# Kernel optimization log

Hardware: AMD Instinct MI355X
Metric: run time of the kernel (lower is better)

## Reference

```python
import jax, jax.numpy as jnp
import numpy as np

D_MODEL = 1024
N_HEADS = 16
HEAD_DIM = 64
SEQ = 2048
BATCH = 2
NEG = -1e9


def rotate_half(t):
    t1, t2 = jnp.split(t, 2, axis=-1)
    return jnp.concatenate([-t2, t1], axis=-1)


def setup_inputs() -> dict:
    key = jax.random.key(0)
    ks = jax.random.split(key, 7)
    std = 0.02
    x = jax.random.normal(ks[0], (BATCH, SEQ, D_MODEL), dtype=jnp.float32)
    # RoPE tables [seq_len, head_dim]
    inv_freq = 1.0 / (10000.0 ** (jnp.arange(0, HEAD_DIM, 2, dtype=jnp.float32) / HEAD_DIM))
    t = jnp.arange(SEQ, dtype=jnp.float32)
    freqs = jnp.outer(t, inv_freq)
    emb = jnp.concatenate([freqs, freqs], axis=-1)
    cos = jnp.cos(emb)
    sin = jnp.sin(emb)
    Wq = std * jax.random.normal(ks[1], (D_MODEL, D_MODEL), dtype=jnp.float32)
    Wk = std * jax.random.normal(ks[2], (D_MODEL, D_MODEL), dtype=jnp.float32)
    Wv = std * jax.random.normal(ks[3], (D_MODEL, D_MODEL), dtype=jnp.float32)
    Wo = std * jax.random.normal(ks[4], (D_MODEL, D_MODEL), dtype=jnp.float32)
    return {"x": x, "cos": cos, "sin": sin, "Wq": Wq, "Wk": Wk, "Wv": Wv, "Wo": Wo}


def reference(x, cos, sin, Wq, Wk, Wv, Wo):
    B, S, _ = x.shape
    scale = 1.0 / np.sqrt(HEAD_DIM)
    # projections (nn.Linear: y = x @ W.T)
    q = (x @ Wq.T).reshape(B, S, N_HEADS, HEAD_DIM).transpose(0, 2, 1, 3)  # [B,H,S,D]
    k = (x @ Wk.T).reshape(B, S, N_HEADS, HEAD_DIM).transpose(0, 2, 1, 3)
    v = (x @ Wv.T).reshape(B, S, N_HEADS, HEAD_DIM).transpose(0, 2, 1, 3)
    # RoPE
    c = cos[None, None, :, :]
    s = sin[None, None, :, :]
    q = q * c + rotate_half(q) * s
    k = k * c + rotate_half(k) * s
    # attention with additive causal mask
    scores = jnp.einsum('bhqd,bhkd->bhqk', q, k) * scale
    causal = jnp.triu(jnp.ones((S, S), dtype=jnp.float32), k=1) * NEG
    scores = scores + causal[None, None]
    attn = jax.nn.softmax(scores, axis=-1)
    out = jnp.einsum('bhqk,bhkd->bhqd', attn, v)
    out = out.transpose(0, 2, 1, 3).reshape(B, S, D_MODEL)
    return out @ Wo.T
```

## Files before the change

kernel.cpp:

```cpp
#include <hip/hip_runtime.h>
#include <hip/hip_bf16.h>
#include <math.h>

#define DM    1024
#define SEQL  2048
#define NB    2
#define MTOT  4096

typedef __attribute__((ext_vector_type(8))) short short8;
typedef __attribute__((ext_vector_type(4))) short short4v;
typedef __attribute__((ext_vector_type(4))) float float4v;

#define GLDS16(g, l) __builtin_amdgcn_global_load_lds( \
    (const __attribute__((address_space(1))) void*)(g), \
    (__attribute__((address_space(3))) void*)(l), 16, 0, 0)

__device__ __forceinline__ short f2bf(float f) {
  union { float f; unsigned u; } c; c.f = f;
  unsigned r = c.u + 0x7FFFu + ((c.u >> 16) & 1u);
  return (short)(r >> 16);
}

__device__ __forceinline__ int packbf(float a, float b) {
  union { float f; unsigned u; } ca, cb; ca.f = a; cb.f = b;
  return (int)__builtin_amdgcn_perm(cb.u + 0x8000u, ca.u + 0x8000u, 0x07060302u);
}

__global__ __launch_bounds__(256) void cvt_all(
    const float* __restrict__ x, const float* __restrict__ wq, const float* __restrict__ wk,
    const float* __restrict__ wv, const float* __restrict__ wo,
    short* __restrict__ xb, short* __restrict__ wqb, short* __restrict__ wkb,
    short* __restrict__ wvb, short* __restrict__ wob) {
  const int n4x = MTOT * DM / 4;
  int i = blockIdx.x * 256 + threadIdx.x;
  const float* s; short* d; int off;
  if (i < n4x) { s = x; d = xb; off = i; }
  else {
    int j = i - n4x;
    int sel = j >> 18;
    off = j & 0x3FFFF;
    s = (sel == 0) ? wq : (sel == 1) ? wk : (sel == 2) ? wv : wo;
    d = (sel == 0) ? wqb : (sel == 1) ? wkb : (sel == 2) ? wvb : wob;
  }
  float4 v = ((const float4*)s)[off];
  short4v o;
  o.x = f2bf(v.x); o.y = f2bf(v.y); o.z = f2bf(v.z); o.w = f2bf(v.w);
  ((short4v*)d)[off] = o;
}

__global__ __launch_bounds__(256, 3) void qkv_kernel(
    const short* __restrict__ A,
    const short* __restrict__ B0, const short* __restrict__ B1, const short* __restrict__ B2,
    short* __restrict__ out0, short* __restrict__ out1, short* __restrict__ out2,
    const float* __restrict__ cosp, const float* __restrict__ sinp)
{
  __shared__ short As[128 * 32];
  __shared__ short Bs[128 * 32];
  const int t = threadIdx.x;
  const int w = t >> 6, lane = t & 63;
  const int quad = lane >> 4, l16 = lane & 15;
  const int wm = w >> 1, wn = w & 1;
  const int bm = blockIdx.y * 128, bn = blockIdx.x * 128;

  const short* Bw = (blockIdx.z == 0) ? B0 : ((blockIdx.z == 1) ? B1 : B2);

  float4v acc[4][4];
#pragma unroll
  for (int i = 0; i < 4; ++i)
#pragma unroll
    for (int j = 0; j < 4; ++j) { float4v z = {0.f, 0.f, 0.f, 0.f}; acc[i][j] = z; }

  for (int k0 = 0; k0 < DM; k0 += 32) {
#pragma unroll
    for (int i = 0; i < 2; ++i) {
      const int c = i * 256 + t;
      const int row = c >> 2, kc = c & 3;
      GLDS16(A  + (size_t)(bm + row) * DM + k0 + kc * 8, As + (i * 256 + w * 64) * 8);
      GLDS16(Bw + (size_t)(bn + row) * DM + k0 + kc * 8, Bs + (i * 256 + w * 64) * 8);
    }
    __syncthreads();
    short8 af[4], bf[4];
#pragma unroll
    for (int mt = 0; mt < 4; ++mt) af[mt] = *(const short8*)&As[(wm * 64 + mt * 16 + l16) * 32 + quad * 8];
#pragma unroll
    for (int nt = 0; nt < 4; ++nt) bf[nt] = *(const short8*)&Bs[(wn * 64 + nt * 16 + l16) * 32 + quad * 8];
#pragma unroll
    for (int mt = 0; mt < 4; ++mt)
#pragma unroll
      for (int nt = 0; nt < 4; ++nt)
        acc[mt][nt] = __builtin_amdgcn_mfma_f32_16x16x32_bf16(af[mt], bf[nt], acc[mt][nt], 0, 0, 0);
    __syncthreads();
  }

  if (blockIdx.z < 2) {
    short* qo = (blockIdx.z == 0) ? out0 : out1;
    const float sc = (blockIdx.z == 0) ? 0.18033688011112042f : 1.0f;
#pragma unroll
    for (int mt = 0; mt < 4; ++mt)
#pragma unroll
      for (int r = 0; r < 4; ++r) {
        int grow = bm + wm * 64 + mt * 16 + quad * 4 + r;
        int s = grow & (SEQL - 1);
        int base = grow * DM + bn + wn * 64;
#pragma unroll
        for (int nt = 0; nt < 2; ++nt) {
          int d1 = nt * 16 + l16;
          float q1 = acc[mt][nt][r], q2 = acc[mt][nt + 2][r];
          float c1 = cosp[s * 64 + d1] * sc,      s1 = sinp[s * 64 + d1] * sc;
          float c2 = cosp[s * 64 + 32 + d1] * sc, s2 = sinp[s * 64 + 32 + d1] * sc;
          qo[base + d1]      = f2bf(q1 * c1 - q2 * s1);
          qo[base + 32 + d1] = f2bf(q2 * c2 + q1 * s2);
        }
      }
  } else {
    short* vo = out2;
#pragma unroll
    for (int mt = 0; mt < 4; ++mt)
#pragma unroll
      for (int nt = 0; nt < 4; ++nt) {
        int gc = bn + wn * 64 + nt * 16 + l16;
        int g0 = bm + wm * 64 + mt * 16 + quad * 4;
        short4v pk;
#pragma unroll
        for (int r = 0; r < 4; ++r) pk[r] = f2bf(acc[mt][nt][r]);
        *(short4v*)&vo[(size_t)gc * MTOT + g0] = pk;
      }
  }
}

#if __has_builtin(__builtin_amdgcn_mfma_f32_16x16x16bf16_1k)
#define HAVE_MFMA16 1
#define MFMA16(a, b, c) __builtin_amdgcn_mfma_f32_16x16x16bf16_1k(a, b, c, 0, 0, 0)
#else
#define HAVE_MFMA16 0
#endif

__global__ __launch_bounds__(256, 2) void attn_kernel(
    const short* __restrict__ Q, const short* __restrict__ K,
    const short* __restrict__ Vt, short* __restrict__ O)
{
  __shared__ short Ks[128 * 64];
  __shared__ short Vs[64 * 128];
  const int t = threadIdx.x;
  const int w = t >> 6, lane = t & 63;
  const int quad = lane >> 4, l16 = lane & 15;
  const int qtA = blockIdx.x;
  const int qtB = 31 - blockIdx.x;
  const int bh = blockIdx.y;
  const int b = bh >> 4, h = bh & 15;
  const int rowbase = b * SEQL;
  const int colbase = h * 64;
  const int nktA = (qtA >> 1) + 1;
  const int nktB = (qtB >> 1) + 1;
  const int qA = qtA * 64 + w * 16 + l16;
  const int qB = qtB * 64 + w * 16 + l16;

  short8 aqA[2], aqB[2];
#pragma unroll
  for (int kk = 0; kk < 2; ++kk) {
    aqA[kk] = *(const short8*)&Q[(size_t)(rowbase + qA) * DM + colbase + kk * 32 + quad * 8];
    aqB[kk] = *(const short8*)&Q[(size_t)(rowbase + qB) * DM + colbase + kk * 32 + quad * 8];
  }

  float4v odA[4], odB[4];
#pragma unroll
  for (int j = 0; j < 4; ++j) { float4v z = {0.f, 0.f, 0.f, 0.f}; odA[j] = z; odB[j] = z; }
  float lA = 0.f, lB = 0.f;

  for (int kt = 0; kt < nktB; ++kt) {
    const bool actA = (kt < nktA);
    const bool diagA = (kt == nktA - 1), diagB = (kt == nktB - 1);
    {
      const short* Kbase = K + (size_t)(rowbase + kt * 128) * DM + colbase;
      const short* Vbase = Vt + (size_t)colbase * MTOT + rowbase + kt * 128;
#pragma unroll
      for (int j = 0; j < 4; ++j) {
        int i = j * 256 + t;
        int n = i >> 3, c = (i & 7) ^ (n & 7);
        GLDS16(Kbase + (size_t)n * DM + c * 8, Ks + (j * 256 + w * 64) * 8);
      }
#pragma unroll
      for (int j = 0; j < 4; ++j) {
        int i = j * 256 + t;
        int d = i >> 4, c = (i & 15) ^ (d & 7);
        GLDS16(Vbase + (size_t)d * MTOT + c * 8, Vs + (j * 256 + w * 64) * 8);
      }
    }
    __syncthreads();

    int pkA[8][2], pkB[8][2];
#pragma unroll
    for (int nt = 0; nt < 8; ++nt) {
      int n = nt * 16 + l16;
      short8 bk0 = *(const short8*)&Ks[(n * 8 + (quad ^ (n & 7))) * 8];
      short8 bk1 = *(const short8*)&Ks[(n * 8 + ((4 + quad) ^ (n & 7))) * 8];
      const int kb = kt * 128 + nt * 16 + quad * 4;
      float4v zz = {0.f, 0.f, 0.f, 0.f};
      float4v sB = __builtin_amdgcn_mfma_f32_16x16x32_bf16(bk0, aqB[0], zz, 0, 0, 0);
      sB = __builtin_amdgcn_mfma_f32_16x16x32_bf16(bk1, aqB[1], sB, 0, 0, 0);
      float pb[4];
#pragma unroll
      for (int r = 0; r < 4; ++r) {
        float p = (diagB && (kb + r > qB)) ? 0.f : __builtin_amdgcn_exp2f(sB[r]);
        lB += p; pb[r] = p;
      }
      pkB[nt][0] = packbf(pb[0], pb[1]);
      pkB[nt][1] = packbf(pb[2], pb[3]);
      if (actA) {
        float4v sA = __builtin_amdgcn_mfma_f32_16x16x32_bf16(bk0, aqA[0], zz, 0, 0, 0);
        sA = __builtin_amdgcn_mfma_f32_16x16x32_bf16(bk1, aqA[1], sA, 0, 0, 0);
        float pa[4];
#pragma unroll
        for (int r = 0; r < 4; ++r) {
          float p = (diagA && (kb + r > qA)) ? 0.f : __builtin_amdgcn_exp2f(sA[r]);
          lA += p; pa[r] = p;
        }
        pkA[nt][0] = packbf(pa[0], pa[1]);
        pkA[nt][1] = packbf(pa[2], pa[3]);
      }
    }

#if HAVE_MFMA16
#pragma unroll
    for (int kk = 0; kk < 8; ++kk) {
      union { int i[2]; short4v s; } ubB, ubA;
      ubB.i[0] = pkB[kk][0]; ubB.i[1] = pkB[kk][1];
      if (actA) { ubA.i[0] = pkA[kk][0]; ubA.i[1] = pkA[kk][1]; }
#pragma unroll
      for (int dt = 0; dt < 4; ++dt) {
        int d = dt * 16 + l16;
        short4v av = *(const short4v*)&Vs[(d * 16 + ((kk * 2 + (quad >> 1)) ^ (d & 7))) * 8 + (quad & 1) * 4];
        odB[dt] = MFMA16(av, ubB.s, odB[dt]);
        if (actA) odA[dt] = MFMA16(av, ubA.s, odA[dt]);
      }
    }
#else
#pragma unroll
    for (int kk = 0; kk < 4; ++kk) {
      union { int i[4]; short8 s; } ubB, ubA;
#pragma unroll
      for (int dj = 0; dj < 4; ++dj) {
        int src = (((quad & 1) * 2 + (dj >> 1)) << 4) + l16;
        int b0 = __shfl(pkB[2 * kk][dj & 1], src);
        int b1 = __shfl(pkB[2 * kk + 1][dj & 1], src);
        ubB.i[dj] = (quad >= 2) ? b1 : b0;
        int a0 = __shfl(pkA[2 * kk][dj & 1], src);
        int a1 = __shfl(pkA[2 * kk + 1][dj & 1], src);
        ubA.i[dj] = (quad >= 2) ? a1 : a0;
      }
#pragma unroll
      for (int dt = 0; dt < 4; ++dt) {
        int d = dt * 16 + l16;
        short8 av = *(const short8*)&Vs[(d * 16 + ((kk * 4 + quad) ^ (d & 7))) * 8];
        odB[dt] = __builtin_amdgcn_mfma_f32_16x16x32_bf16(av, ubB.s, odB[dt], 0, 0, 0);
        if (actA) odA[dt] = __builtin_amdgcn_mfma_f32_16x16x32_bf16(av, ubA.s, odA[dt], 0, 0, 0);
      }
    }
#endif
    __syncthreads();
  }

  lA += __shfl_xor(lA, 16); lA += __shfl_xor(lA, 32);
  lB += __shfl_xor(lB, 16); lB += __shfl_xor(lB, 32);
  const float iA = 1.f / lA, iB = 1.f / lB;

#pragma unroll
  for (int dt = 0; dt < 4; ++dt) {
    short4v sa, sb;
#pragma unroll
    for (int r = 0; r < 4; ++r) { sa[r] = f2bf(odA[dt][r] * iA); sb[r] = f2bf(odB[dt][r] * iB); }
    int col = colbase + dt * 16 + quad * 4;
    *(short4v*)&O[(size_t)(rowbase + qA) * DM + col] = sa;
    *(short4v*)&O[(size_t)(rowbase + qB) * DM + col] = sb;
  }
}

__global__ __launch_bounds__(256, 2) void gemm_out(
    const short* __restrict__ A, const short* __restrict__ B,
    float* __restrict__ out)
{
  __shared__ short As[128 * 32];
  __shared__ short Bs[64 * 32];
  const int t = threadIdx.x;
  const int w = t >> 6, lane = t & 63;
  const int quad = lane >> 4, l16 = lane & 15;
  const int wm = w >> 1, wn = w & 1;
  const int bm = blockIdx.y * 128, bn = blockIdx.x * 64;

  float4v acc[4][2];
#pragma unroll
  for (int i = 0; i < 4; ++i)
#pragma unroll
    for (int j = 0; j < 2; ++j) { float4v z = {0.f, 0.f, 0.f, 0.f}; acc[i][j] = z; }

  for (int k0 = 0; k0 < DM; k0 += 32) {
#pragma unroll
    for (int i = 0; i < 2; ++i) {
      const int c = i * 256 + t;
      const int row = c >> 2, kc = c & 3;
      GLDS16(A + (size_t)(bm + row) * DM + k0 + kc * 8, As + (i * 256 + w * 64) * 8);
    }
    {
      const int row = t >> 2, kc = t & 3;
      GLDS16(B + (size_t)(bn + row) * DM + k0 + kc * 8, Bs + (w * 64) * 8);
    }
    __syncthreads();
    short8 af[4], bf[2];
#pragma unroll
    for (int mt = 0; mt < 4; ++mt) af[mt] = *(const short8*)&As[(wm * 64 + mt * 16 + l16) * 32 + quad * 8];
#pragma unroll
    for (int nt = 0; nt < 2; ++nt) bf[nt] = *(const short8*)&Bs[(wn * 32 + nt * 16 + l16) * 32 + quad * 8];
#pragma unroll
    for (int mt = 0; mt < 4; ++mt)
#pragma unroll
      for (int nt = 0; nt < 2; ++nt)
        acc[mt][nt] = __builtin_amdgcn_mfma_f32_16x16x32_bf16(af[mt], bf[nt], acc[mt][nt], 0, 0, 0);
    __syncthreads();
  }

#pragma unroll
  for (int mt = 0; mt < 4; ++mt)
#pragma unroll
    for (int nt = 0; nt < 2; ++nt)
#pragma unroll
      for (int r = 0; r < 4; ++r) {
        int grow = bm + wm * 64 + mt * 16 + quad * 4 + r;
        int gcol = bn + wn * 32 + nt * 16 + l16;
        out[(size_t)grow * DM + gcol] = acc[mt][nt][r];
      }
}

extern "C" void kernel_launch(void* const* d_in, const int* in_sizes, int n_in,
                              void* d_out, int out_size, void* d_ws, size_t ws_size,
                              hipStream_t stream) {
  const float* x    = (const float*)d_in[0];
  const float* cosp = (const float*)d_in[1];
  const float* sinp = (const float*)d_in[2];
  const float* Wq   = (const float*)d_in[3];
  const float* Wk   = (const float*)d_in[4];
  const float* Wv   = (const float*)d_in[5];
  const float* Wo   = (const float*)d_in[6];

  char* ws = (char*)d_ws;
  const size_t XB = (size_t)MTOT * DM * 2;
  const size_t WB = (size_t)DM * DM * 2;
  short* xb    = (short*)(ws);
  short* wqb   = (short*)(ws + XB);
  short* wkb   = (short*)(ws + XB + 1 * WB);
  short* wvb   = (short*)(ws + XB + 2 * WB);
  short* wob   = (short*)(ws + XB + 3 * WB);
  short* Qb    = (short*)(ws + XB + 4 * WB);
  short* Kb    = (short*)(ws + XB + 4 * WB + XB);
  short* Vtb   = (short*)(ws + XB + 4 * WB + 2 * XB);
  short* attnb = xb;

  const int n4tot = (MTOT * DM + 4 * DM * DM) / 4;
  hipLaunchKernelGGL(cvt_all, dim3(n4tot / 256), dim3(256), 0, stream,
                     x, Wq, Wk, Wv, Wo, xb, wqb, wkb, wvb, wob);

  hipLaunchKernelGGL(qkv_kernel, dim3(DM / 128, MTOT / 128, 3), dim3(256), 0, stream,
                     xb, wqb, wkb, wvb, Qb, Kb, Vtb, cosp, sinp);

  hipLaunchKernelGGL(attn_kernel, dim3(16, NB * 16), dim3(256), 0, stream,
                     Qb, Kb, Vtb, attnb);

  hipLaunchKernelGGL(gemm_out, dim3(DM / 64, MTOT / 128), dim3(256), 0, stream,
                     attnb, wob, (float*)d_out);
}
```

Before: 200.9 us.

## Split paired attention tiles into separate blocks and deepen QKV GEMM k-step

```diff
diff --git a/kernel.cpp b/kernel.cpp
--- a/kernel.cpp
+++ b/kernel.cpp
@@ -54,8 +54,8 @@
     short* __restrict__ out0, short* __restrict__ out1, short* __restrict__ out2,
     const float* __restrict__ cosp, const float* __restrict__ sinp)
 {
-  __shared__ short As[128 * 32];
-  __shared__ short Bs[128 * 32];
+  __shared__ short As[128 * 64];
+  __shared__ short Bs[128 * 64];
   const int t = threadIdx.x;
   const int w = t >> 6, lane = t & 63;
   const int quad = lane >> 4, l16 = lane & 15;
@@ -70,25 +70,30 @@
 #pragma unroll
     for (int j = 0; j < 4; ++j) { float4v z = {0.f, 0.f, 0.f, 0.f}; acc[i][j] = z; }
 
-  for (int k0 = 0; k0 < DM; k0 += 32) {
-#pragma unroll
-    for (int i = 0; i < 2; ++i) {
-      const int c = i * 256 + t;
-      const int row = c >> 2, kc = c & 3;
-      GLDS16(A  + (size_t)(bm + row) * DM + k0 + kc * 8, As + (i * 256 + w * 64) * 8);
-      GLDS16(Bw + (size_t)(bn + row) * DM + k0 + kc * 8, Bs + (i * 256 + w * 64) * 8);
-    }
-    __syncthreads();
-    short8 af[4], bf[4];
-#pragma unroll
-    for (int mt = 0; mt < 4; ++mt) af[mt] = *(const short8*)&As[(wm * 64 + mt * 16 + l16) * 32 + quad * 8];
-#pragma unroll
-    for (int nt = 0; nt < 4; ++nt) bf[nt] = *(const short8*)&Bs[(wn * 64 + nt * 16 + l16) * 32 + quad * 8];
-#pragma unroll
-    for (int mt = 0; mt < 4; ++mt)
+  for (int k0 = 0; k0 < DM; k0 += 64) {
+#pragma unroll
+    for (int j = 0; j < 4; ++j) {
+      const int i = j * 256 + t;
+      const int row = i >> 3, c = i & 7;
+      GLDS16(A  + (size_t)(bm + row) * DM + k0 + c * 8, As + (j * 256 + w * 64) * 8);
+      GLDS16(Bw + (size_t)(bn + row) * DM + k0 + c * 8, Bs + (j * 256 + w * 64) * 8);
+    }
+    __syncthreads();
+#pragma unroll
+    for (int kk2 = 0; kk2 < 2; ++kk2) {
+      short8 af[4], bf[4];
+#pragma unroll
+      for (int mt = 0; mt < 4; ++mt)
+        af[mt] = *(const short8*)&As[(wm * 64 + mt * 16 + l16) * 64 + kk2 * 32 + quad * 8];
 #pragma unroll
       for (int nt = 0; nt < 4; ++nt)
-        acc[mt][nt] = __builtin_amdgcn_mfma_f32_16x16x32_bf16(af[mt], bf[nt], acc[mt][nt], 0, 0, 0);
+        bf[nt] = *(const short8*)&Bs[(wn * 64 + nt * 16 + l16) * 64 + kk2 * 32 + quad * 8];
+#pragma unroll
+      for (int mt = 0; mt < 4; ++mt)
+#pragma unroll
+        for (int nt = 0; nt < 4; ++nt)
+          acc[mt][nt] = __builtin_amdgcn_mfma_f32_16x16x32_bf16(af[mt], bf[nt], acc[mt][nt], 0, 0, 0);
+    }
     __syncthreads();
   }
 
@@ -135,7 +140,7 @@
 #define HAVE_MFMA16 0
 #endif
 
-__global__ __launch_bounds__(256, 2) void attn_kernel(
+__global__ __launch_bounds__(256, 4) void attn_kernel(
     const short* __restrict__ Q, const short* __restrict__ K,
     const short* __restrict__ Vt, short* __restrict__ O)
 {
@@ -144,32 +149,26 @@
   const int t = threadIdx.x;
   const int w = t >> 6, lane = t & 63;
   const int quad = lane >> 4, l16 = lane & 15;
-  const int qtA = blockIdx.x;
-  const int qtB = 31 - blockIdx.x;
+  const int qt = 31 - blockIdx.x;
   const int bh = blockIdx.y;
   const int b = bh >> 4, h = bh & 15;
   const int rowbase = b * SEQL;
   const int colbase = h * 64;
-  const int nktA = (qtA >> 1) + 1;
-  const int nktB = (qtB >> 1) + 1;
-  const int qA = qtA * 64 + w * 16 + l16;
-  const int qB = qtB * 64 + w * 16 + l16;
-
-  short8 aqA[2], aqB[2];
-#pragma unroll
-  for (int kk = 0; kk < 2; ++kk) {
-    aqA[kk] = *(const short8*)&Q[(size_t)(rowbase + qA) * DM + colbase + kk * 32 + quad * 8];
-    aqB[kk] = *(const short8*)&Q[(size_t)(rowbase + qB) * DM + colbase + kk * 32 + quad * 8];
-  }
-
-  float4v odA[4], odB[4];
-#pragma unroll
-  for (int j = 0; j < 4; ++j) { float4v z = {0.f, 0.f, 0.f, 0.f}; odA[j] = z; odB[j] = z; }
-  float lA = 0.f, lB = 0.f;
-
-  for (int kt = 0; kt < nktB; ++kt) {
-    const bool actA = (kt < nktA);
-    const bool diagA = (kt == nktA - 1), diagB = (kt == nktB - 1);
+  const int nkt = (qt >> 1) + 1;
+  const int q = qt * 64 + w * 16 + l16;
+
+  short8 aq[2];
+#pragma unroll
+  for (int kk = 0; kk < 2; ++kk)
+    aq[kk] = *(const short8*)&Q[(size_t)(rowbase + q) * DM + colbase + kk * 32 + quad * 8];
+
+  float4v od[4];
+#pragma unroll
+  for (int j = 0; j < 4; ++j) { float4v z = {0.f, 0.f, 0.f, 0.f}; od[j] = z; }
+  float lsum = 0.f;
+
+  for (int kt = 0; kt < nkt; ++kt) {
+    const bool diag = (kt == nkt - 1);
     {
       const short* Kbase = K + (size_t)(rowbase + kt * 128) * DM + colbase;
       const short* Vbase = Vt + (size_t)colbase * MTOT + rowbase + kt * 128;
@@ -188,7 +187,7 @@
     }
     __syncthreads();
 
-    int pkA[8][2], pkB[8][2];
+    int pk[8][2];
 #pragma unroll
     for (int nt = 0; nt < 8; ++nt) {
       int n = nt * 16 + l16;
@@ -196,82 +195,63 @@
       short8 bk1 = *(const short8*)&Ks[(n * 8 + ((4 + quad) ^ (n & 7))) * 8];
       const int kb = kt * 128 + nt * 16 + quad * 4;
       float4v zz = {0.f, 0.f, 0.f, 0.f};
-      float4v sB = __builtin_amdgcn_mfma_f32_16x16x32_bf16(bk0, aqB[0], zz, 0, 0, 0);
-      sB = __builtin_amdgcn_mfma_f32_16x16x32_bf16(bk1, aqB[1], sB, 0, 0, 0);
-      float pb[4];
+      float4v s = __builtin_amdgcn_mfma_f32_16x16x32_bf16(bk0, aq[0], zz, 0, 0, 0);
+      s = __builtin_amdgcn_mfma_f32_16x16x32_bf16(bk1, aq[1], s, 0, 0, 0);
+      float pr[4];
 #pragma unroll
       for (int r = 0; r < 4; ++r) {
-        float p = (diagB && (kb + r > qB)) ? 0.f : __builtin_amdgcn_exp2f(sB[r]);
-        lB += p; pb[r] = p;
-      }
-      pkB[nt][0] = packbf(pb[0], pb[1]);
-      pkB[nt][1] = packbf(pb[2], pb[3]);
-      if (actA) {
-        float4v sA = __builtin_amdgcn_mfma_f32_16x16x32_bf16(bk0, aqA[0], zz, 0, 0, 0);
-        sA = __builtin_amdgcn_mfma_f32_16x16x32_bf16(bk1, aqA[1], sA, 0, 0, 0);
-        float pa[4];
-#pragma unroll
-        for (int r = 0; r < 4; ++r) {
-          float p = (diagA && (kb + r > qA)) ? 0.f : __builtin_amdgcn_exp2f(sA[r]);
-          lA += p; pa[r] = p;
-        }
-        pkA[nt][0] = packbf(pa[0], pa[1]);
-        pkA[nt][1] = packbf(pa[2], pa[3]);
-      }
+        float p = (diag && (kb + r > q)) ? 0.f : __builtin_amdgcn_exp2f(s[r]);
+        lsum += p; pr[r] = p;
+      }
+      pk[nt][0] = packbf(pr[0], pr[1]);
+      pk[nt][1] = packbf(pr[2], pr[3]);
     }
 
 #if HAVE_MFMA16
 #pragma unroll
     for (int kk = 0; kk < 8; ++kk) {
-      union { int i[2]; short4v s; } ubB, ubA;
-      ubB.i[0] = pkB[kk][0]; ubB.i[1] = pkB[kk][1];
-      if (actA) { ubA.i[0] = pkA[kk][0]; ubA.i[1] = pkA[kk][1]; }
+      union { int i[2]; short4v s; } ub;
+      ub.i[0] = pk[kk][0]; ub.i[1] = pk[kk][1];
 #pragma unroll
       for (int dt = 0; dt < 4; ++dt) {
         int d = dt * 16 + l16;
         short4v av = *(const short4v*)&Vs[(d * 16 + ((kk * 2 + (quad >> 1)) ^ (d & 7))) * 8 + (quad & 1) * 4];
-        odB[dt] = MFMA16(av, ubB.s, odB[dt]);
-        if (actA) odA[dt] = MFMA16(av, ubA.s, odA[dt]);
+        od[dt] = MFMA16(av, ub.s, od[dt]);
       }
     }
 #else
 #pragma unroll
     for (int kk = 0; kk < 4; ++kk) {
-      union { int i[4]; short8 s; } ubB, ubA;
+      union { int i[4]; short8 s; } ub;
 #pragma unroll
       for (int dj = 0; dj < 4; ++dj) {
         int src = (((quad & 1) * 2 + (dj >> 1)) << 4) + l16;
-        int b0 = __shfl(pkB[2 * kk][dj & 1], src);
-        int b1 = __shfl(pkB[2 * kk + 1][dj & 1], src);
-        ubB.i[dj] = (quad >= 2) ? b1 : b0;
-        int a0 = __shfl(pkA[2 * kk][dj & 1], src);
-        int a1 = __shfl(pkA[2 * kk + 1][dj & 1], src);
-        ubA.i[dj] = (quad >= 2) ? a1 : a0;
+        int b0 = __shfl(pk[2 * kk][dj & 1], src);
+        int b1 = __shfl(pk[2 * kk + 1][dj & 1], src);
+        ub.i[dj] = (quad >= 2) ? b1 : b0;
       }
 #pragma unroll
       for (int dt = 0; dt < 4; ++dt) {
         int d = dt * 16 + l16;
         short8 av = *(const short8*)&Vs[(d * 16 + ((kk * 4 + quad) ^ (d & 7))) * 8];
-        odB[dt] = __builtin_amdgcn_mfma_f32_16x16x32_bf16(av, ubB.s, odB[dt], 0, 0, 0);
-        if (actA) odA[dt] = __builtin_amdgcn_mfma_f32_16x16x32_bf16(av, ubA.s, odA[dt], 0, 0, 0);
+        od[dt] = __builtin_amdgcn_mfma_f32_16x16x32_bf16(av, ub.s, od[dt], 0, 0, 0);
       }
     }
 #endif
     __syncthreads();
   }
 
-  lA += __shfl_xor(lA, 16); lA += __shfl_xor(lA, 32);
-  lB += __shfl_xor(lB, 16); lB += __shfl_xor(lB, 32);
-  const float iA = 1.f / lA, iB = 1.f / lB;
+  lsum += __shfl_xor(lsum, 16);
+  lsum += __shfl_xor(lsum, 32);
+  const float inv = 1.f / lsum;
 
 #pragma unroll
   for (int dt = 0; dt < 4; ++dt) {
-    short4v sa, sb;
-#pragma unroll
-    for (int r = 0; r < 4; ++r) { sa[r] = f2bf(odA[dt][r] * iA); sb[r] = f2bf(odB[dt][r] * iB); }
+    short4v sv;
+#pragma unroll
+    for (int r = 0; r < 4; ++r) sv[r] = f2bf(od[dt][r] * inv);
     int col = colbase + dt * 16 + quad * 4;
-    *(short4v*)&O[(size_t)(rowbase + qA) * DM + col] = sa;
-    *(short4v*)&O[(size_t)(rowbase + qB) * DM + col] = sb;
+    *(short4v*)&O[(size_t)(rowbase + q) * DM + col] = sv;
   }
 }
 
@@ -361,7 +341,7 @@
   hipLaunchKernelGGL(qkv_kernel, dim3(DM / 128, MTOT / 128, 3), dim3(256), 0, stream,
                      xb, wqb, wkb, wvb, Qb, Kb, Vtb, cosp, sinp);
 
-  hipLaunchKernelGGL(attn_kernel, dim3(16, NB * 16), dim3(256), 0, stream,
+  hipLaunchKernelGGL(attn_kernel, dim3(32, NB * 16), dim3(256), 0, stream,
                      Qb, Kb, Vtb, attnb);
 
   hipLaunchKernelGGL(gemm_out, dim3(DM / 64, MTOT / 128), dim3(256), 0, stream,
```

Result: no change. 203.6 us (+1.3%).

## Double-buffer LDS tiles in QKV, attention and output GEMM kernels

Applied to the files above, without the earlier changes.

```diff
diff --git a/kernel.cpp b/kernel.cpp
--- a/kernel.cpp
+++ b/kernel.cpp
@@ -54,8 +54,8 @@
     short* __restrict__ out0, short* __restrict__ out1, short* __restrict__ out2,
     const float* __restrict__ cosp, const float* __restrict__ sinp)
 {
-  __shared__ short As[128 * 32];
-  __shared__ short Bs[128 * 32];
+  __shared__ short As[2][128 * 32];
+  __shared__ short Bs[2][128 * 32];
   const int t = threadIdx.x;
   const int w = t >> 6, lane = t & 63;
   const int quad = lane >> 4, l16 = lane & 15;
@@ -70,26 +70,32 @@
 #pragma unroll
     for (int j = 0; j < 4; ++j) { float4v z = {0.f, 0.f, 0.f, 0.f}; acc[i][j] = z; }
 
-  for (int k0 = 0; k0 < DM; k0 += 32) {
+  const int srow = t >> 2, skc = t & 3;
+  auto stage = [&](int k0, int p) {
 #pragma unroll
     for (int i = 0; i < 2; ++i) {
-      const int c = i * 256 + t;
-      const int row = c >> 2, kc = c & 3;
-      GLDS16(A  + (size_t)(bm + row) * DM + k0 + kc * 8, As + (i * 256 + w * 64) * 8);
-      GLDS16(Bw + (size_t)(bn + row) * DM + k0 + kc * 8, Bs + (i * 256 + w * 64) * 8);
-    }
+      const int row = (i * 256 + t) >> 2, kc = (i * 256 + t) & 3;
+      GLDS16(A  + (size_t)(bm + row) * DM + k0 + kc * 8, &As[p][(i * 256 + w * 64) * 8]);
+      GLDS16(Bw + (size_t)(bn + row) * DM + k0 + kc * 8, &Bs[p][(i * 256 + w * 64) * 8]);
+    }
+  };
+  (void)srow; (void)skc;
+
+  stage(0, 0);
+  for (int ki = 0; ki < 32; ++ki) {
+    const int p = ki & 1;
     __syncthreads();
+    if (ki < 31) stage((ki + 1) * 32, p ^ 1);
     short8 af[4], bf[4];
 #pragma unroll
-    for (int mt = 0; mt < 4; ++mt) af[mt] = *(const short8*)&As[(wm * 64 + mt * 16 + l16) * 32 + quad * 8];
-#pragma unroll
-    for (int nt = 0; nt < 4; ++nt) bf[nt] = *(const short8*)&Bs[(wn * 64 + nt * 16 + l16) * 32 + quad * 8];
+    for (int mt = 0; mt < 4; ++mt) af[mt] = *(const short8*)&As[p][(wm * 64 + mt * 16 + l16) * 32 + quad * 8];
+#pragma unroll
+    for (int nt = 0; nt < 4; ++nt) bf[nt] = *(const short8*)&Bs[p][(wn * 64 + nt * 16 + l16) * 32 + quad * 8];
 #pragma unroll
     for (int mt = 0; mt < 4; ++mt)
 #pragma unroll
       for (int nt = 0; nt < 4; ++nt)
         acc[mt][nt] = __builtin_amdgcn_mfma_f32_16x16x32_bf16(af[mt], bf[nt], acc[mt][nt], 0, 0, 0);
-    __syncthreads();
   }
 
   if (blockIdx.z < 2) {
@@ -139,8 +145,8 @@
     const short* __restrict__ Q, const short* __restrict__ K,
     const short* __restrict__ Vt, short* __restrict__ O)
 {
-  __shared__ short Ks[128 * 64];
-  __shared__ short Vs[64 * 128];
+  __shared__ short Ks[2][128 * 64];
+  __shared__ short Vs[2][64 * 128];
   const int t = threadIdx.x;
   const int w = t >> 6, lane = t & 63;
   const int quad = lane >> 4, l16 = lane & 15;
@@ -167,33 +173,41 @@
   for (int j = 0; j < 4; ++j) { float4v z = {0.f, 0.f, 0.f, 0.f}; odA[j] = z; odB[j] = z; }
   float lA = 0.f, lB = 0.f;
 
+  auto stage = [&](int kt, int p) {
+    const short* Kbase = K + (size_t)(rowbase + kt * 128) * DM + colbase;
+    const short* Vbase = Vt + (size_t)colbase * MTOT + rowbase + kt * 128;
+    short* kd = &Ks[p][0];
+    short* vd = &Vs[p][0];
+#pragma unroll
+    for (int j = 0; j < 4; ++j) {
+      int i = j * 256 + t;
+      int n = i >> 3, c = (i & 7) ^ (n & 7);
+      GLDS16(Kbase + (size_t)n * DM + c * 8, kd + (j * 256 + w * 64) * 8);
+    }
+#pragma unroll
+    for (int j = 0; j < 4; ++j) {
+      int i = j * 256 + t;
+      int d = i >> 4, c = (i & 15) ^ (d & 7);
+      GLDS16(Vbase + (size_t)d * MTOT + c * 8, vd + (j * 256 + w * 64) * 8);
+    }
+  };
+
+  stage(0, 0);
   for (int kt = 0; kt < nktB; ++kt) {
+    const int p = kt & 1;
+    __syncthreads();
+    if (kt + 1 < nktB) stage(kt + 1, p ^ 1);
+    const short* ks = &Ks[p][0];
+    const short* vs = &Vs[p][0];
     const bool actA = (kt < nktA);
     const bool diagA = (kt == nktA - 1), diagB = (kt == nktB - 1);
-    {
-      const short* Kbase = K + (size_t)(rowbase + kt * 128) * DM + colbase;
-      const short* Vbase = Vt + (size_t)colbase * MTOT + rowbase + kt * 128;
-#pragma unroll
-      for (int j = 0; j < 4; ++j) {
-        int i = j * 256 + t;
-        int n = i >> 3, c = (i & 7) ^ (n & 7);
-        GLDS16(Kbase + (size_t)n * DM + c * 8, Ks + (j * 256 + w * 64) * 8);
-      }
-#pragma unroll
-      for (int j = 0; j < 4; ++j) {
-        int i = j * 256 + t;
-        int d = i >> 4, c = (i & 15) ^ (d & 7);
-        GLDS16(Vbase + (size_t)d * MTOT + c * 8, Vs + (j * 256 + w * 64) * 8);
-      }
-    }
-    __syncthreads();
 
     int pkA[8][2], pkB[8][2];
 #pragma unroll
     for (int nt = 0; nt < 8; ++nt) {
       int n = nt * 16 + l16;
-      short8 bk0 = *(const short8*)&Ks[(n * 8 + (quad ^ (n & 7))) * 8];
-      short8 bk1 = *(const short8*)&Ks[(n * 8 + ((4 + quad) ^ (n & 7))) * 8];
+      short8 bk0 = *(const short8*)&ks[(n * 8 + (quad ^ (n & 7))) * 8];
+      short8 bk1 = *(const short8*)&ks[(n * 8 + ((4 + quad) ^ (n & 7))) * 8];
       const int kb = kt * 128 + nt * 16 + quad * 4;
       float4v zz = {0.f, 0.f, 0.f, 0.f};
       float4v sB = __builtin_amdgcn_mfma_f32_16x16x32_bf16(bk0, aqB[0], zz, 0, 0, 0);
@@ -201,8 +215,8 @@
       float pb[4];
 #pragma unroll
       for (int r = 0; r < 4; ++r) {
-        float p = (diagB && (kb + r > qB)) ? 0.f : __builtin_amdgcn_exp2f(sB[r]);
-        lB += p; pb[r] = p;
+        float pv = (diagB && (kb + r > qB)) ? 0.f : __builtin_amdgcn_exp2f(sB[r]);
+        lB += pv; pb[r] = pv;
       }
       pkB[nt][0] = packbf(pb[0], pb[1]);
       pkB[nt][1] = packbf(pb[2], pb[3]);
@@ -212,8 +226,8 @@
         float pa[4];
 #pragma unroll
         for (int r = 0; r < 4; ++r) {
-          float p = (diagA && (kb + r > qA)) ? 0.f : __builtin_amdgcn_exp2f(sA[r]);
-          lA += p; pa[r] = p;
+          float pv = (diagA && (kb + r > qA)) ? 0.f : __builtin_amdgcn_exp2f(sA[r]);
+          lA += pv; pa[r] = pv;
         }
         pkA[nt][0] = packbf(pa[0], pa[1]);
         pkA[nt][1] = packbf(pa[2], pa[3]);
@@ -229,7 +243,7 @@
 #pragma unroll
       for (int dt = 0; dt < 4; ++dt) {
         int d = dt * 16 + l16;
-        short4v av = *(const short4v*)&Vs[(d * 16 + ((kk * 2 + (quad >> 1)) ^ (d & 7))) * 8 + (quad & 1) * 4];
+        short4v av = *(const short4v*)&vs[(d * 16 + ((kk * 2 + (quad >> 1)) ^ (d & 7))) * 8 + (quad & 1) * 4];
         odB[dt] = MFMA16(av, ubB.s, odB[dt]);
         if (actA) odA[dt] = MFMA16(av, ubA.s, odA[dt]);
       }
@@ -251,13 +265,12 @@
 #pragma unroll
       for (int dt = 0; dt < 4; ++dt) {
         int d = dt * 16 + l16;
-        short8 av = *(const short8*)&Vs[(d * 16 + ((kk * 4 + quad) ^ (d & 7))) * 8];
+        short8 av = *(const short8*)&vs[(d * 16 + ((kk * 4 + quad) ^ (d & 7))) * 8];
         odB[dt] = __builtin_amdgcn_mfma_f32_16x16x32_bf16(av, ubB.s, odB[dt], 0, 0, 0);
         if (actA) odA[dt] = __builtin_amdgcn_mfma_f32_16x16x32_bf16(av, ubA.s, odA[dt], 0, 0, 0);
       }
     }
 #endif
-    __syncthreads();
   }
 
   lA += __shfl_xor(lA, 16); lA += __shfl_xor(lA, 32);
@@ -279,8 +292,8 @@
     const short* __restrict__ A, const short* __restrict__ B,
     float* __restrict__ out)
 {
-  __shared__ short As[128 * 32];
-  __shared__ short Bs[64 * 32];
+  __shared__ short As[2][128 * 32];
+  __shared__ short Bs[2][64 * 32];
   const int t = threadIdx.x;
   const int w = t >> 6, lane = t & 63;
   const int quad = lane >> 4, l16 = lane & 15;
@@ -293,29 +306,33 @@
 #pragma unroll
     for (int j = 0; j < 2; ++j) { float4v z = {0.f, 0.f, 0.f, 0.f}; acc[i][j] = z; }
 
-  for (int k0 = 0; k0 < DM; k0 += 32) {
+  auto stage = [&](int k0, int p) {
 #pragma unroll
     for (int i = 0; i < 2; ++i) {
-      const int c = i * 256 + t;
-      const int row = c >> 2, kc = c & 3;
-      GLDS16(A + (size_t)(bm + row) * DM + k0 + kc * 8, As + (i * 256 + w * 64) * 8);
+      const int row = (i * 256 + t) >> 2, kc = (i * 256 + t) & 3;
+      GLDS16(A + (size_t)(bm + row) * DM + k0 + kc * 8, &As[p][(i * 256 + w * 64) * 8]);
     }
     {
       const int row = t >> 2, kc = t & 3;
-      GLDS16(B + (size_t)(bn + row) * DM + k0 + kc * 8, Bs + (w * 64) * 8);
-    }
+      GLDS16(B + (size_t)(bn + row) * DM + k0 + kc * 8, &Bs[p][(w * 64) * 8]);
+    }
+  };
+
+  stage(0, 0);
+  for (int ki = 0; ki < 32; ++ki) {
+    const int p = ki & 1;
     __syncthreads();
+    if (ki < 31) stage((ki + 1) * 32, p ^ 1);
     short8 af[4], bf[2];
 #pragma unroll
-    for (int mt = 0; mt < 4; ++mt) af[mt] = *(const short8*)&As[(wm * 64 + mt * 16 + l16) * 32 + quad * 8];
-#pragma unroll
-    for (int nt = 0; nt < 2; ++nt) bf[nt] = *(const short8*)&Bs[(wn * 32 + nt * 16 + l16) * 32 + quad * 8];
+    for (int mt = 0; mt < 4; ++mt) af[mt] = *(const short8*)&As[p][(wm * 64 + mt * 16 + l16) * 32 + quad * 8];
+#pragma unroll
+    for (int nt = 0; nt < 2; ++nt) bf[nt] = *(const short8*)&Bs[p][(wn * 32 + nt * 16 + l16) * 32 + quad * 8];
 #pragma unroll
     for (int mt = 0; mt < 4; ++mt)
 #pragma unroll
       for (int nt = 0; nt < 2; ++nt)
         acc[mt][nt] = __builtin_amdgcn_mfma_f32_16x16x32_bf16(af[mt], bf[nt], acc[mt][nt], 0, 0, 0);
-    __syncthreads();
   }
 
 #pragma unroll
```

Result: no change. 201.3 us (+0.2%).
